# Optimization experiments

Measured on AMD Instinct MI355X. Metric: run time of the kernel, lower is better.

## Reference

```python
import jax, jax.numpy as jnp
import numpy as np

D_MODEL = 1024
N_HEADS = 16
D_K = D_MODEL // N_HEADS


def setup_inputs() -> dict:
    key = jax.random.key(0)
    ks = jax.random.split(key, 9)
    s = 1.0 / np.sqrt(D_MODEL)
    return {
        "x": jax.random.normal(ks[0], (4, 2048, D_MODEL), dtype=jnp.float32),
        "Wq": jax.random.normal(ks[1], (D_MODEL, D_MODEL), dtype=jnp.float32) * s,
        "bq": jax.random.normal(ks[2], (D_MODEL,), dtype=jnp.float32) * 0.01,
        "Wk": jax.random.normal(ks[3], (D_MODEL, D_MODEL), dtype=jnp.float32) * s,
        "bk": jax.random.normal(ks[4], (D_MODEL,), dtype=jnp.float32) * 0.01,
        "Wv": jax.random.normal(ks[5], (D_MODEL, D_MODEL), dtype=jnp.float32) * s,
        "bv": jax.random.normal(ks[6], (D_MODEL,), dtype=jnp.float32) * 0.01,
        "Wo": jax.random.normal(ks[7], (D_MODEL, D_MODEL), dtype=jnp.float32) * s,
        "bo": jax.random.normal(ks[8], (D_MODEL,), dtype=jnp.float32) * 0.01,
    }


def reference(x, Wq, bq, Wk, bk, Wv, bv, Wo, bo):
    B, S, _ = x.shape
    # projections (torch Linear: x @ W.T + b; here W stored as [in, out])
    q = (x @ Wq + bq).reshape(B, S, N_HEADS, D_K).transpose(0, 2, 1, 3)  # [B,H,S,Dk]
    k = (x @ Wk + bk).reshape(B, S, N_HEADS, D_K).transpose(0, 2, 1, 3)
    v = (x @ Wv + bv).reshape(B, S, N_HEADS, D_K).transpose(0, 2, 1, 3)
    scale = 1.0 / np.sqrt(D_K).astype(np.float32)
    scores = jnp.einsum("bhsd,bhtd->bhst", q, k) * scale  # [B,H,S,S]
    attn = jax.nn.softmax(scores, axis=-1)
    ctx = jnp.einsum("bhst,bhtd->bhsd", attn, v)  # [B,H,S,Dk]
    ctx = ctx.transpose(0, 2, 1, 3).reshape(B, S, D_MODEL)
    return ctx @ Wo + bo
```

## Files before the change

kernel.cpp:

```cpp
#include <hip/hip_runtime.h>
#include <math.h>

#define DMODEL 1024
#define NHEADS 16
#define DKDIM  64
#define SEQLEN 2048
#define NBATCH 4
#define MTOT   (NBATCH * SEQLEN)

typedef __attribute__((ext_vector_type(8)))  short short8;
typedef __attribute__((ext_vector_type(4)))  float f32x4;
typedef __attribute__((ext_vector_type(16))) float f32x16;

__device__ __forceinline__ unsigned short f2bf(float x) {
    unsigned u = __builtin_bit_cast(unsigned, x);
    unsigned r = (u + 0x7fffu + ((u >> 16) & 1u)) >> 16;
    return (unsigned short)r;
}

__device__ __forceinline__ void gload16(const void* g, void* l) {
    __builtin_amdgcn_global_load_lds(
        (const __attribute__((address_space(1))) void*)g,
        (__attribute__((address_space(3))) void*)l, 16, 0, 0);
}

__global__ __launch_bounds__(256)
void convert_x_kernel(const float* __restrict__ x, unsigned short* __restrict__ xb)
{
    const size_t i = ((size_t)blockIdx.x * 256 + threadIdx.x) * 8;
    const float4 a = *(const float4*)&x[i];
    const float4 b = *(const float4*)&x[i + 4];
    union { unsigned short u[8]; uint4 q; } p;
    p.u[0] = f2bf(a.x); p.u[1] = f2bf(a.y); p.u[2] = f2bf(a.z); p.u[3] = f2bf(a.w);
    p.u[4] = f2bf(b.x); p.u[5] = f2bf(b.y); p.u[6] = f2bf(b.z); p.u[7] = f2bf(b.w);
    *(uint4*)&xb[i] = p.q;
}

__global__ __launch_bounds__(256)
void convert_w_kernel(const float* __restrict__ W0, const float* __restrict__ W1,
                      const float* __restrict__ W2, const float* __restrict__ W3,
                      unsigned short* __restrict__ wt)
{
    const int z = blockIdx.z;
    const float* W = (z == 0) ? W0 : (z == 1) ? W1 : (z == 2) ? W2 : W3;
    unsigned short* dst = wt + (size_t)z * DMODEL * DMODEL;
    const int n0 = blockIdx.x * 64, k0 = blockIdx.y * 64;
    __shared__ float T[64][65];
    const int t = threadIdx.x;
    const int r0 = t >> 4, c0 = (t & 15) << 2;
#pragma unroll
    for (int u = 0; u < 4; ++u) {
        const float4 wv = *(const float4*)&W[(size_t)(k0 + r0 + u * 16) * DMODEL + n0 + c0];
        T[c0 + 0][r0 + u * 16] = wv.x;
        T[c0 + 1][r0 + u * 16] = wv.y;
        T[c0 + 2][r0 + u * 16] = wv.z;
        T[c0 + 3][r0 + u * 16] = wv.w;
    }
    __syncthreads();
    const int rn = t >> 2, ck = (t & 3) << 4;
    union { unsigned short u16[16]; uint4 q[2]; } pk;
#pragma unroll
    for (int e = 0; e < 16; ++e) pk.u16[e] = f2bf(T[rn][ck + e]);
    *(uint4*)&dst[(size_t)(n0 + rn) * DMODEL + k0 + ck]     = pk.q[0];
    *(uint4*)&dst[(size_t)(n0 + rn) * DMODEL + k0 + ck + 8] = pk.q[1];
}

template<int OMODE>
__device__ __forceinline__
void gemm_core(const unsigned short* __restrict__ A, const unsigned short* __restrict__ Bt,
               const float* __restrict__ bias, void* __restrict__ outv, const float scl)
{
    __shared__ __align__(16) char As[128 * 128];
    __shared__ __align__(16) char Bs[128 * 128];

    const int t  = threadIdx.x;
    const int l  = t & 63, w = t >> 6;
    const int g  = (l >> 4), lr = l & 15;
    const int wr = w >> 1, wc = w & 1;
    const int swz = (lr & 7) << 4;

    const int flat = (blockIdx.y << 3) | blockIdx.x;
    const int sid  = ((flat & 7) << 6) | (flat >> 3);
    const int m0 = (sid >> 3) << 7;
    const int n0 = (sid & 7) << 7;

    f32x4 acc[4][4];
#pragma unroll
    for (int i = 0; i < 4; ++i)
#pragma unroll
        for (int j = 0; j < 4; ++j) acc[i][j] = (f32x4){0.f, 0.f, 0.f, 0.f};

    for (int k0 = 0; k0 < DMODEL; k0 += 64) {
        __syncthreads();
#pragma unroll
        for (int qd = 0; qd < 4; ++qd) {
            const int o   = (t + qd * 256) << 4;
            const int row = o >> 7;
            const int c   = (o & 127) ^ ((row & 7) << 4);
            gload16((const char*)A  + (((size_t)(m0 + row) * DMODEL + k0) << 1) + c, As + o);
            gload16((const char*)Bt + (((size_t)(n0 + row) * DMODEL + k0) << 1) + c, Bs + o);
        }
        __syncthreads();

        short8 af[4][2], bf[4][2];
#pragma unroll
        for (int i = 0; i < 4; ++i)
#pragma unroll
            for (int kk = 0; kk < 2; ++kk) {
                const int off = (kk * 64 + g * 16) ^ swz;
                af[i][kk] = *(const short8*)(As + (wr * 64 + i * 16 + lr) * 128 + off);
                bf[i][kk] = *(const short8*)(Bs + (wc * 64 + i * 16 + lr) * 128 + off);
            }
        __builtin_amdgcn_s_setprio(1);
#pragma unroll
        for (int kk = 0; kk < 2; ++kk)
#pragma unroll
            for (int i = 0; i < 4; ++i)
#pragma unroll
                for (int j = 0; j < 4; ++j)
                    acc[i][j] = __builtin_amdgcn_mfma_f32_16x16x32_bf16(
                        af[i][kk], bf[j][kk], acc[i][j], 0, 0, 0);
        __builtin_amdgcn_s_setprio(0);
    }

    float bj[4];
#pragma unroll
    for (int j = 0; j < 4; ++j) bj[j] = bias[n0 + wc * 64 + j * 16 + lr];

#pragma unroll
    for (int i = 0; i < 4; ++i)
#pragma unroll
        for (int j = 0; j < 4; ++j) {
            const int mb = m0 + wr * 64 + i * 16 + g * 4;
            const int n  = n0 + wc * 64 + j * 16 + lr;
            float v[4];
#pragma unroll
            for (int r = 0; r < 4; ++r) v[r] = (acc[i][j][r] + bj[j]) * scl;
            if (OMODE == 0) {
                unsigned short* outp = (unsigned short*)outv;
#pragma unroll
                for (int r = 0; r < 4; ++r)
                    outp[(size_t)(mb + r) * DMODEL + n] = f2bf(v[r]);
            } else if (OMODE == 1) {
                unsigned short* outp = (unsigned short*)outv;
                const int b = mb >> 11, s = mb & (SEQLEN - 1);
                const size_t idx = (((size_t)(b * NHEADS + (n >> 6)) * DKDIM + (n & 63)) << 11) + s;
                uint2 pk;
                pk.x = (unsigned)f2bf(v[0]) | ((unsigned)f2bf(v[1]) << 16);
                pk.y = (unsigned)f2bf(v[2]) | ((unsigned)f2bf(v[3]) << 16);
                *(uint2*)&outp[idx] = pk;
            } else {
                float* outp = (float*)outv;
#pragma unroll
                for (int r = 0; r < 4; ++r)
                    outp[(size_t)(mb + r) * DMODEL + n] = v[r];
            }
        }
}

#define QSCALE 0.1803368801111137f

__global__ __launch_bounds__(256)
void qkv_gemm_kernel(const unsigned short* __restrict__ xb, const unsigned short* __restrict__ wt,
                     const float* __restrict__ bq, const float* __restrict__ bk,
                     const float* __restrict__ bv,
                     unsigned short* __restrict__ Qb, unsigned short* __restrict__ Kb,
                     unsigned short* __restrict__ Vt)
{
    if (blockIdx.z == 0)      gemm_core<0>(xb, wt,                      bq, Qb, QSCALE);
    else if (blockIdx.z == 1) gemm_core<0>(xb, wt + DMODEL * DMODEL,     bk, Kb, 1.0f);
    else                      gemm_core<1>(xb, wt + 2 * DMODEL * DMODEL, bv, Vt, 1.0f);
}

__global__ __launch_bounds__(256)
void out_gemm_kernel(const unsigned short* __restrict__ ctx, const unsigned short* __restrict__ wt,
                     const float* __restrict__ bo, float* __restrict__ out)
{
    gemm_core<2>(ctx, wt + 3 * DMODEL * DMODEL, bo, out, 1.0f);
}

__device__ __forceinline__
void attn_body(const char* __restrict__ Kbuf, const char* __restrict__ Vbuf,
               const short8 (&qf)[4], const short8 ones,
               f32x16 (&po)[2], f32x16& po_l,
               int q32, int hi, int swz)
{
#pragma unroll
    for (int hf = 0; hf < 2; ++hf) {
        f32x16 s;
#pragma unroll
        for (int r = 0; r < 16; ++r) s[r] = 0.f;
        short8 kf[4];
#pragma unroll
        for (int kk = 0; kk < 4; ++kk)
            kf[kk] = *(const short8*)(Kbuf + (hf * 32 + q32) * 128 + ((kk * 32 + hi * 16) ^ swz));
        __builtin_amdgcn_s_setprio(1);
#pragma unroll
        for (int kk = 0; kk < 4; ++kk)
            s = __builtin_amdgcn_mfma_f32_32x32x16_bf16(kf[kk], qf[kk], s, 0, 0, 0);
        __builtin_amdgcn_s_setprio(0);

#pragma unroll
        for (int r = 0; r < 16; ++r) s[r] = __builtin_amdgcn_exp2f(s[r]);

        short8 pf[2];
#pragma unroll
        for (int j = 0; j < 2; ++j) {
            const int bse = j * 8;
            unsigned wA0, wA1, wB0, wB1;
            asm("v_cvt_pk_bf16_f32 %0, %1, %2" : "=v"(wA0) : "v"(s[bse + 0]), "v"(s[bse + 1]));
            asm("v_cvt_pk_bf16_f32 %0, %1, %2" : "=v"(wA1) : "v"(s[bse + 2]), "v"(s[bse + 3]));
            asm("v_cvt_pk_bf16_f32 %0, %1, %2" : "=v"(wB0) : "v"(s[bse + 4]), "v"(s[bse + 5]));
            asm("v_cvt_pk_bf16_f32 %0, %1, %2" : "=v"(wB1) : "v"(s[bse + 6]), "v"(s[bse + 7]));
            asm volatile("v_permlane32_swap_b32 %0, %1" : "+v"(wA0), "+v"(wB0));
            asm volatile("v_permlane32_swap_b32 %0, %1" : "+v"(wA1), "+v"(wB1));
            union { unsigned u[4]; short8 s8; } pk;
            pk.u[0] = wA0; pk.u[1] = wA1; pk.u[2] = wB0; pk.u[3] = wB1;
            pf[j] = pk.s8;
        }

        short8 vf0[2], vf1[2];
#pragma unroll
        for (int j = 0; j < 2; ++j) {
            const int ks = hf * 2 + j;
            vf0[j] = *(const short8*)(Vbuf + q32 * 128 + ((ks * 32 + hi * 16) ^ swz));
            vf1[j] = *(const short8*)(Vbuf + (32 + q32) * 128 + ((ks * 32 + hi * 16) ^ swz));
        }
        __builtin_amdgcn_s_setprio(1);
#pragma unroll
        for (int j = 0; j < 2; ++j) {
            po[0] = __builtin_amdgcn_mfma_f32_32x32x16_bf16(vf0[j], pf[j], po[0], 0, 0, 0);
            po[1] = __builtin_amdgcn_mfma_f32_32x32x16_bf16(vf1[j], pf[j], po[1], 0, 0, 0);
            po_l  = __builtin_amdgcn_mfma_f32_32x32x16_bf16(ones,   pf[j], po_l,  0, 0, 0);
        }
        __builtin_amdgcn_s_setprio(0);
    }
}

__global__ __launch_bounds__(512)
void attn_kernel(const unsigned short* __restrict__ Qb, const unsigned short* __restrict__ Kb,
                 const unsigned short* __restrict__ Vt, unsigned short* __restrict__ ctx)
{
    __shared__ __align__(16) char smem[49152];

    const int t   = threadIdx.x;
    const int l   = t & 63, w = t >> 6;
    const int q32 = l & 31, hi = l >> 5;
    const int swz = (q32 & 7) << 4;

    const int flat = (blockIdx.y << 3) | blockIdx.x;
    const int sid  = ((flat & 7) << 6) | (flat >> 3);
    const int qt = sid & 7;
    const int bh = sid >> 3;
    const int b  = bh >> 4, h = bh & 15;
    const int coln = h * DKDIM;

    const size_t qrow  = (size_t)b * SEQLEN + qt * 256 + w * 32 + q32;
    const size_t krow0 = (size_t)b * SEQLEN;
    const size_t vbase = (size_t)(b * NHEADS + h) * DKDIM * SEQLEN;

    short8 qf[4];
#pragma unroll
    for (int kk = 0; kk < 4; ++kk)
        qf[kk] = *(const short8*)(Qb + qrow * DMODEL + coln + kk * 16 + hi * 8);

    short8 ones;
#pragma unroll
    for (int e = 0; e < 8; ++e) ones[e] = (short)0x3F80;

    f32x16 po[2], po_l;
#pragma unroll
    for (int r = 0; r < 16; ++r) { po[0][r] = 0.f; po[1][r] = 0.f; po_l[r] = 0.f; }

    const int so   = t << 4;
    const int srow = so >> 7;
    const int sc_  = (so & 127) ^ ((srow & 7) << 4);

#define STAGE(bufidx, kt)                                                                    \
    do {                                                                                     \
        gload16((const char*)Kb + (((krow0 + (kt) * 64 + srow) * DMODEL + coln) << 1) + sc_, \
                smem + (bufidx) * 8192 + so);                                                \
        gload16((const char*)Vt + ((vbase + (size_t)srow * SEQLEN + (kt) * 64) << 1) + sc_,  \
                smem + 24576 + (bufidx) * 8192 + so);                                        \
    } while (0)

    STAGE(0, 0);
    STAGE(1, 1);

#pragma unroll 1
    for (int kt = 0; kt < 31; ++kt) {
        asm volatile("s_waitcnt vmcnt(2)" ::: "memory");
        __builtin_amdgcn_s_barrier();
        if (kt + 2 < 32) STAGE((kt + 2) % 3, kt + 2);
        const int buf = kt % 3;
        attn_body(smem + buf * 8192, smem + 24576 + buf * 8192,
                  qf, ones, po, po_l, q32, hi, swz);
    }
    asm volatile("s_waitcnt vmcnt(0)" ::: "memory");
    __builtin_amdgcn_s_barrier();
    attn_body(smem + 8192, smem + 24576 + 8192, qf, ones, po, po_l, q32, hi, swz);

    __syncthreads();

    const float inv = 1.0f / po_l[0];
    char* T = smem + w * 4096;
#pragma unroll
    for (int i = 0; i < 2; ++i)
#pragma unroll
        for (int g4 = 0; g4 < 4; ++g4) {
            const int d0 = i * 32 + g4 * 8 + hi * 4;
            uint2 pk;
            pk.x = (unsigned)f2bf(po[i][g4 * 4 + 0] * inv) | ((unsigned)f2bf(po[i][g4 * 4 + 1] * inv) << 16);
            pk.y = (unsigned)f2bf(po[i][g4 * 4 + 2] * inv) | ((unsigned)f2bf(po[i][g4 * 4 + 3] * inv) << 16);
            *(uint2*)(T + ((q32 * 128 + d0 * 2) ^ swz)) = pk;
        }
    __syncthreads();
#pragma unroll
    for (int pass = 0; pass < 4; ++pass) {
        const int o   = (l + pass * 64) << 4;
        const int row = o >> 7;
        const int c   = o & 127;
        const uint4 val = *(const uint4*)(T + (o ^ ((row & 7) << 4)));
        const size_t token = (size_t)b * SEQLEN + qt * 256 + w * 32 + row;
        *(uint4*)&ctx[token * DMODEL + coln + (c >> 1)] = val;
    }
#undef STAGE
}

extern "C" void kernel_launch(void* const* d_in, const int* in_sizes, int n_in,
                              void* d_out, int out_size, void* d_ws, size_t ws_size,
                              hipStream_t stream)
{
    const float* x  = (const float*)d_in[0];
    const float* Wq = (const float*)d_in[1];
    const float* bq = (const float*)d_in[2];
    const float* Wk = (const float*)d_in[3];
    const float* bk = (const float*)d_in[4];
    const float* Wv = (const float*)d_in[5];
    const float* bv = (const float*)d_in[6];
    const float* Wo = (const float*)d_in[7];
    const float* bo = (const float*)d_in[8];
    float* out = (float*)d_out;

    const size_t NE = (size_t)MTOT * DMODEL;
    unsigned short* xb  = (unsigned short*)d_ws;
    unsigned short* wt  = xb  + NE;
    unsigned short* Qb  = wt  + (size_t)4 * DMODEL * DMODEL;
    unsigned short* Kb  = Qb  + NE;
    unsigned short* Vt  = Kb  + NE;
    unsigned short* ctx = Vt  + NE;

    convert_x_kernel<<<dim3(NE / (256 * 8)), 256, 0, stream>>>(x, xb);
    convert_w_kernel<<<dim3(16, 16, 4), 256, 0, stream>>>(Wq, Wk, Wv, Wo, wt);
    qkv_gemm_kernel<<<dim3(8, 64, 3), 256, 0, stream>>>(xb, wt, bq, bk, bv, Qb, Kb, Vt);
    attn_kernel<<<dim3(SEQLEN / 256, NBATCH * NHEADS), dim3(512), 0, stream>>>(Qb, Kb, Vt, ctx);
    out_gemm_kernel<<<dim3(8, 64), 256, 0, stream>>>(ctx, wt, bo, out);
}
```

Baseline: 178.6 us.

## Software-pipeline attention: overlap QK/exp of next tile with PV of previous

Restructures the attention inner loop so the QK^T scores and exp/convert for key tile k+1 are computed before the PV MMA for tile k, letting exponentials overlap with matrix work. The LDS ring grows from three to four K/V stages (64 KB shared) to hold the extra in-flight tile. Launch bounds add a minimum of 4 blocks per CU. This raises register pressure (two probability fragment sets, two score tiles live) and LDS use, which may limit occupancy.

After: 387.6 us. 117% more time.

```diff
diff --git a/kernel.cpp b/kernel.cpp
--- a/kernel.cpp
+++ b/kernel.cpp
@@ -180,68 +180,72 @@
 }
 
 __device__ __forceinline__
-void attn_body(const char* __restrict__ Kbuf, const char* __restrict__ Vbuf,
-               const short8 (&qf)[4], const short8 ones,
-               f32x16 (&po)[2], f32x16& po_l,
-               int q32, int hi, int swz)
-{
-#pragma unroll
-    for (int hf = 0; hf < 2; ++hf) {
-        f32x16 s;
-#pragma unroll
-        for (int r = 0; r < 16; ++r) s[r] = 0.f;
-        short8 kf[4];
-#pragma unroll
-        for (int kk = 0; kk < 4; ++kk)
-            kf[kk] = *(const short8*)(Kbuf + (hf * 32 + q32) * 128 + ((kk * 32 + hi * 16) ^ swz));
+void qk_full(const char* __restrict__ Kbuf, const short8 (&qf)[4],
+             f32x16& s0, f32x16& s1, int q32, int hi, int swz)
+{
+#pragma unroll
+    for (int r = 0; r < 16; ++r) { s0[r] = 0.f; s1[r] = 0.f; }
+    short8 kf0[4], kf1[4];
+#pragma unroll
+    for (int kk = 0; kk < 4; ++kk) {
+        kf0[kk] = *(const short8*)(Kbuf + q32 * 128 + ((kk * 32 + hi * 16) ^ swz));
+        kf1[kk] = *(const short8*)(Kbuf + (32 + q32) * 128 + ((kk * 32 + hi * 16) ^ swz));
+    }
+    __builtin_amdgcn_s_setprio(1);
+#pragma unroll
+    for (int kk = 0; kk < 4; ++kk)
+        s0 = __builtin_amdgcn_mfma_f32_32x32x16_bf16(kf0[kk], qf[kk], s0, 0, 0, 0);
+#pragma unroll
+    for (int kk = 0; kk < 4; ++kk)
+        s1 = __builtin_amdgcn_mfma_f32_32x32x16_bf16(kf1[kk], qf[kk], s1, 0, 0, 0);
+    __builtin_amdgcn_s_setprio(0);
+}
+
+__device__ __forceinline__
+void exp_cvt(f32x16& s0, f32x16& s1, short8 (&pf)[4])
+{
+#pragma unroll
+    for (int r = 0; r < 16; ++r) s0[r] = __builtin_amdgcn_exp2f(s0[r]);
+#pragma unroll
+    for (int r = 0; r < 16; ++r) s1[r] = __builtin_amdgcn_exp2f(s1[r]);
+#pragma unroll
+    for (int ks = 0; ks < 4; ++ks) {
+        const f32x16& st = (ks < 2) ? s0 : s1;
+        const int bse = (ks & 1) * 8;
+        unsigned wA0, wA1, wB0, wB1;
+        asm("v_cvt_pk_bf16_f32 %0, %1, %2" : "=v"(wA0) : "v"(st[bse + 0]), "v"(st[bse + 1]));
+        asm("v_cvt_pk_bf16_f32 %0, %1, %2" : "=v"(wA1) : "v"(st[bse + 2]), "v"(st[bse + 3]));
+        asm("v_cvt_pk_bf16_f32 %0, %1, %2" : "=v"(wB0) : "v"(st[bse + 4]), "v"(st[bse + 5]));
+        asm("v_cvt_pk_bf16_f32 %0, %1, %2" : "=v"(wB1) : "v"(st[bse + 6]), "v"(st[bse + 7]));
+        asm volatile("v_permlane32_swap_b32 %0, %1" : "+v"(wA0), "+v"(wB0));
+        asm volatile("v_permlane32_swap_b32 %0, %1" : "+v"(wA1), "+v"(wB1));
+        union { unsigned u[4]; short8 s8; } pk;
+        pk.u[0] = wA0; pk.u[1] = wA1; pk.u[2] = wB0; pk.u[3] = wB1;
+        pf[ks] = pk.s8;
+    }
+}
+
+__device__ __forceinline__
+void pv_full(const char* __restrict__ Vbuf, const short8 (&pf)[4], const short8 ones,
+             f32x16 (&po)[2], f32x16& po_l, int q32, int hi, int swz)
+{
+#pragma unroll
+    for (int ks = 0; ks < 4; ++ks) {
+        const short8 vf0 = *(const short8*)(Vbuf + q32 * 128 + ((ks * 32 + hi * 16) ^ swz));
+        const short8 vf1 = *(const short8*)(Vbuf + (32 + q32) * 128 + ((ks * 32 + hi * 16) ^ swz));
         __builtin_amdgcn_s_setprio(1);
-#pragma unroll
-        for (int kk = 0; kk < 4; ++kk)
-            s = __builtin_amdgcn_mfma_f32_32x32x16_bf16(kf[kk], qf[kk], s, 0, 0, 0);
+        po[0] = __builtin_amdgcn_mfma_f32_32x32x16_bf16(vf0, pf[ks], po[0], 0, 0, 0);
+        po[1] = __builtin_amdgcn_mfma_f32_32x32x16_bf16(vf1, pf[ks], po[1], 0, 0, 0);
+        po_l  = __builtin_amdgcn_mfma_f32_32x32x16_bf16(ones, pf[ks], po_l,  0, 0, 0);
         __builtin_amdgcn_s_setprio(0);
-
-#pragma unroll
-        for (int r = 0; r < 16; ++r) s[r] = __builtin_amdgcn_exp2f(s[r]);
-
-        short8 pf[2];
-#pragma unroll
-        for (int j = 0; j < 2; ++j) {
-            const int bse = j * 8;
-            unsigned wA0, wA1, wB0, wB1;
-            asm("v_cvt_pk_bf16_f32 %0, %1, %2" : "=v"(wA0) : "v"(s[bse + 0]), "v"(s[bse + 1]));
-            asm("v_cvt_pk_bf16_f32 %0, %1, %2" : "=v"(wA1) : "v"(s[bse + 2]), "v"(s[bse + 3]));
-            asm("v_cvt_pk_bf16_f32 %0, %1, %2" : "=v"(wB0) : "v"(s[bse + 4]), "v"(s[bse + 5]));
-            asm("v_cvt_pk_bf16_f32 %0, %1, %2" : "=v"(wB1) : "v"(s[bse + 6]), "v"(s[bse + 7]));
-            asm volatile("v_permlane32_swap_b32 %0, %1" : "+v"(wA0), "+v"(wB0));
-            asm volatile("v_permlane32_swap_b32 %0, %1" : "+v"(wA1), "+v"(wB1));
-            union { unsigned u[4]; short8 s8; } pk;
-            pk.u[0] = wA0; pk.u[1] = wA1; pk.u[2] = wB0; pk.u[3] = wB1;
-            pf[j] = pk.s8;
-        }
-
-        short8 vf0[2], vf1[2];
-#pragma unroll
-        for (int j = 0; j < 2; ++j) {
-            const int ks = hf * 2 + j;
-            vf0[j] = *(const short8*)(Vbuf + q32 * 128 + ((ks * 32 + hi * 16) ^ swz));
-            vf1[j] = *(const short8*)(Vbuf + (32 + q32) * 128 + ((ks * 32 + hi * 16) ^ swz));
-        }
-        __builtin_amdgcn_s_setprio(1);
-#pragma unroll
-        for (int j = 0; j < 2; ++j) {
-            po[0] = __builtin_amdgcn_mfma_f32_32x32x16_bf16(vf0[j], pf[j], po[0], 0, 0, 0);
-            po[1] = __builtin_amdgcn_mfma_f32_32x32x16_bf16(vf1[j], pf[j], po[1], 0, 0, 0);
-            po_l  = __builtin_amdgcn_mfma_f32_32x32x16_bf16(ones,   pf[j], po_l,  0, 0, 0);
-        }
-        __builtin_amdgcn_s_setprio(0);
-    }
-}
-
-__global__ __launch_bounds__(512)
+    }
+}
+
+__global__ __launch_bounds__(512, 4)
 void attn_kernel(const unsigned short* __restrict__ Qb, const unsigned short* __restrict__ Kb,
                  const unsigned short* __restrict__ Vt, unsigned short* __restrict__ ctx)
 {
-    __shared__ __align__(16) char smem[49152];
+    __shared__ __align__(16) char smem[65536];
 
     const int t   = threadIdx.x;
     const int l   = t & 63, w = t >> 6;
@@ -276,29 +280,51 @@
     const int srow = so >> 7;
     const int sc_  = (so & 127) ^ ((srow & 7) << 4);
 
+#define KBUF(i) (smem + (i) * 8192)
+#define VBUF(i) (smem + 32768 + (i) * 8192)
 #define STAGE(bufidx, kt)                                                                    \
     do {                                                                                     \
         gload16((const char*)Kb + (((krow0 + (kt) * 64 + srow) * DMODEL + coln) << 1) + sc_, \
-                smem + (bufidx) * 8192 + so);                                                \
+                KBUF(bufidx) + so);                                                          \
         gload16((const char*)Vt + ((vbase + (size_t)srow * SEQLEN + (kt) * 64) << 1) + sc_,  \
-                smem + 24576 + (bufidx) * 8192 + so);                                        \
+                VBUF(bufidx) + so);                                                          \
     } while (0)
+
+    f32x16 s0, s1;
+    short8 pfA[4], pfB[4];
 
     STAGE(0, 0);
     STAGE(1, 1);
 
+    asm volatile("s_waitcnt vmcnt(2)" ::: "memory");
+    __builtin_amdgcn_s_barrier();
+    STAGE(2, 2);
+    qk_full(KBUF(0), qf, s0, s1, q32, hi, swz);
+    exp_cvt(s0, s1, pfA);
+
 #pragma unroll 1
-    for (int kt = 0; kt < 31; ++kt) {
+    for (int kt = 1; kt < 31; kt += 2) {
         asm volatile("s_waitcnt vmcnt(2)" ::: "memory");
         __builtin_amdgcn_s_barrier();
-        if (kt + 2 < 32) STAGE((kt + 2) % 3, kt + 2);
-        const int buf = kt % 3;
-        attn_body(smem + buf * 8192, smem + 24576 + buf * 8192,
-                  qf, ones, po, po_l, q32, hi, swz);
-    }
+        STAGE((kt + 2) & 3, kt + 2);
+        qk_full(KBUF(kt & 3), qf, s0, s1, q32, hi, swz);
+        exp_cvt(s0, s1, pfB);
+        pv_full(VBUF((kt - 1) & 3), pfA, ones, po, po_l, q32, hi, swz);
+
+        asm volatile("s_waitcnt vmcnt(2)" ::: "memory");
+        __builtin_amdgcn_s_barrier();
+        if (kt + 3 < 32) STAGE((kt + 3) & 3, kt + 3);
+        qk_full(KBUF((kt + 1) & 3), qf, s0, s1, q32, hi, swz);
+        exp_cvt(s0, s1, pfA);
+        pv_full(VBUF(kt & 3), pfB, ones, po, po_l, q32, hi, swz);
+    }
+
     asm volatile("s_waitcnt vmcnt(0)" ::: "memory");
     __builtin_amdgcn_s_barrier();
-    attn_body(smem + 8192, smem + 24576 + 8192, qf, ones, po, po_l, q32, hi, swz);
+    qk_full(KBUF(3), qf, s0, s1, q32, hi, swz);
+    exp_cvt(s0, s1, pfB);
+    pv_full(VBUF(2), pfA, ones, po, po_l, q32, hi, swz);
+    pv_full(VBUF(3), pfB, ones, po, po_l, q32, hi, swz);
 
     __syncthreads();
 
@@ -325,6 +351,8 @@
         *(uint4*)&ctx[token * DMODEL + coln + (c >> 1)] = val;
     }
 #undef STAGE
+#undef KBUF
+#undef VBUF
 }
 
 extern "C" void kernel_launch(void* const* d_in, const int* in_sizes, int n_in,
```
